# Kernel optimization log

Hardware: AMD Instinct MI355X
Metric: run time of the kernel (lower is better)

Reference implementation:

```python
import jax, jax.numpy as jnp
import numpy as np

EPS_PHI = 1e-18  # weight assigned to neighbors outside the support radius


def setup_inputs() -> dict:
    key = jax.random.key(0)
    k1, k2, k3, k4 = jax.random.split(key, 4)
    N, P, K = 2, 100000, 60
    points = jax.random.normal(k1, (N, P, 3), dtype=jnp.float32)
    v = jax.random.normal(k2, (N, P, K, 3), dtype=jnp.float32)
    vn = jax.random.normal(k3, (N, P, K, 3), dtype=jnp.float32)
    # squared support radii: positive, bounded away from zero
    sr = jax.random.uniform(k4, (N, P, K), dtype=jnp.float32) + 0.1
    return {"points": points, "v": v, "vn": vn, "sr": sr}


def reference(points, v, vn, sr):
    # points: (N,P,3); v,vn: (N,P,K,3); sr: (N,P,K)
    p_v = points[:, :, None, :] - v                      # (N,P,K,3)
    dists = jnp.sum(p_v * p_v, axis=-1)                  # (N,P,K) squared distances
    inside = dists < sr                                  # (N,P,K)
    w = 1.0 - dists / sr
    phi_v = jnp.where(inside, (w * w) * (w * w), EPS_PHI)  # quartic kernel weight
    v_to_p_dot_n = jnp.sum(vn * p_v, axis=-1)            # (N,P,K)
    sdf = jnp.sum(phi_v * v_to_p_dot_n, axis=-1) / jnp.sum(phi_v, axis=-1)  # (N,P)
    return jnp.sum(sdf * sdf, axis=-1)                   # (N,)
```

## Files before the change

### kernel.cpp

```cpp
#include <hip/hip_runtime.h>

#define RED_THREADS 512

__global__ __launch_bounds__(256) void sdf_main(
    const float* __restrict__ points,
    const float* __restrict__ v,
    const float* __restrict__ vn,
    const float* __restrict__ sr,
    float* __restrict__ ws,
    int NP, int P, int slots, int slotStride)
{
    constexpr int K = 60;
    __shared__ float4 sv[4][45];
    __shared__ float4 sn[4][45];
    __shared__ float4 ss[4][15];

    const int w     = threadIdx.x >> 6;
    const int lane  = threadIdx.x & 63;
    const int point = blockIdx.x * 4 + w;
    const bool active = point < NP;

    float px = 0.f, py = 0.f, pz = 0.f;
    if (active) {
        const float4* v4 = (const float4*)(v  + (size_t)point * (K * 3));
        const float4* n4 = (const float4*)(vn + (size_t)point * (K * 3));
        const float4* s4 = (const float4*)(sr + (size_t)point * K);
        float4 rv, rn, rs;
        if (lane < 45) rv = v4[lane];
        if (lane < 45) rn = n4[lane];
        if (lane < 15) rs = s4[lane];
        px = points[point * 3 + 0];
        py = points[point * 3 + 1];
        pz = points[point * 3 + 2];
        if (lane < 45) sv[w][lane] = rv;
        if (lane < 45) sn[w][lane] = rn;
        if (lane < 15) ss[w][lane] = rs;
    }
    __syncthreads();

    float num = 0.f, den = 0.f;
    if (active && lane < K) {
        const float* vf = (const float*)sv[w];
        const float* nf = (const float*)sn[w];
        const float* sf = (const float*)ss[w];
        const float vx = vf[3 * lane + 0];
        const float vy = vf[3 * lane + 1];
        const float vz = vf[3 * lane + 2];
        const float nx = nf[3 * lane + 0];
        const float ny = nf[3 * lane + 1];
        const float nz = nf[3 * lane + 2];
        const float s  = sf[lane];

        const float dx = px - vx;
        const float dy = py - vy;
        const float dz = pz - vz;
        const float d2 = dx * dx + dy * dy + dz * dz;
        const float wq = 1.0f - d2 / s;
        const float w2 = wq * wq;
        const float phi = (d2 < s) ? (w2 * w2) : 1e-18f;
        const float dot = nx * dx + ny * dy + nz * dz;
        num = phi * dot;
        den = phi;
    }

    #pragma unroll
    for (int off = 32; off >= 1; off >>= 1) {
        num += __shfl_xor(num, off, 64);
        den += __shfl_xor(den, off, 64);
    }

    if (active && lane == 0) {
        const float sdf = num / den;
        const int n    = point / P;
        const int slot = point & (slots - 1);
        atomicAdd(&ws[slot * slotStride + n], sdf * sdf);
    }
}

__global__ __launch_bounds__(RED_THREADS) void sdf_reduce(
    const float* __restrict__ ws, float* __restrict__ out,
    int N, int slots, int slotStride)
{
    __shared__ float sm0[RED_THREADS];
    __shared__ float sm1[RED_THREADS];
    const int tid = threadIdx.x;
    float a = 0.f, b = 0.f;
    for (int s = tid; s < slots; s += RED_THREADS) {
        a += ws[s * slotStride + 0];
        if (N > 1) b += ws[s * slotStride + 1];
    }
    sm0[tid] = a;
    sm1[tid] = b;
    __syncthreads();
    #pragma unroll
    for (int s = RED_THREADS / 2; s >= 1; s >>= 1) {
        if (tid < s) {
            sm0[tid] += sm0[tid + s];
            sm1[tid] += sm1[tid + s];
        }
        __syncthreads();
    }
    if (tid == 0) {
        out[0] = sm0[0];
        if (N > 1) out[1] = sm1[0];
    }
}

extern "C" void kernel_launch(void* const* d_in, const int* in_sizes, int n_in,
                              void* d_out, int out_size, void* d_ws, size_t ws_size,
                              hipStream_t stream) {
    const float* points = (const float*)d_in[0];
    const float* v      = (const float*)d_in[1];
    const float* vn     = (const float*)d_in[2];
    const float* sr     = (const float*)d_in[3];
    float* out = (float*)d_out;
    float* ws  = (float*)d_ws;

    const int NP = in_sizes[0] / 3;
    const int N  = out_size;
    const int P  = NP / N;

    int slots = 512, slotStride = 16;
    if (ws_size < (size_t)(slots * slotStride * sizeof(float))) {
        slots = 256; slotStride = 2;
    }

    hipMemsetAsync(ws, 0, (size_t)slots * slotStride * sizeof(float), stream);

    const int blocks = (NP + 3) / 4;
    sdf_main<<<blocks, 256, 0, stream>>>(points, v, vn, sr, ws, NP, P,
                                         slots, slotStride);
    sdf_reduce<<<1, RED_THREADS, 0, stream>>>(ws, out, N, slots, slotStride);
}
```

Before: 327.0 us.

## Use persistent waves with register-prefetched point groups and per-wave accumulation

Replaces the one-point-per-wave grid with a fixed grid of 1280 blocks. Each wave walks a contiguous range of points in groups of four, prefetching the next group's v/vn/sr into registers while computing the current group from shared memory. Per-batch partial sums are kept in registers and flushed with a few atomics per wave, cutting atomic traffic. The added block-level syncs and the serialized per-point shuffle reductions may limit how much latency is hidden. With cpw around 20, the final group per wave is partial.

```diff
diff --git a/kernel.cpp b/kernel.cpp
--- a/kernel.cpp
+++ b/kernel.cpp
@@ -1,79 +1,136 @@
 #include <hip/hip_runtime.h>
 
+#define WPB 4
+#define BT  256
+#define G   4
+#define MAXN 4
 #define RED_THREADS 512
 
-__global__ __launch_bounds__(256) void sdf_main(
+__global__ __launch_bounds__(BT) void sdf_main(
     const float* __restrict__ points,
     const float* __restrict__ v,
     const float* __restrict__ vn,
     const float* __restrict__ sr,
     float* __restrict__ ws,
-    int NP, int P, int slots, int slotStride)
+    int NP, int P, int cpw, int iters, int slots, int slotStride)
 {
-    constexpr int K = 60;
-    __shared__ float4 sv[4][45];
-    __shared__ float4 sn[4][45];
-    __shared__ float4 ss[4][15];
+    constexpr int K   = 60;
+    constexpr int VF4 = 45;
+    constexpr int SF4 = 15;
+    __shared__ float4 buf[WPB][G * (2 * VF4 + SF4)];
 
-    const int w     = threadIdx.x >> 6;
-    const int lane  = threadIdx.x & 63;
-    const int point = blockIdx.x * 4 + w;
-    const bool active = point < NP;
+    const int w      = threadIdx.x >> 6;
+    const int lane   = threadIdx.x & 63;
+    const int waveId = blockIdx.x * WPB + w;
+    const int p0     = waveId * cpw;
+    const int pEnd   = min(NP, p0 + cpw);
 
-    float px = 0.f, py = 0.f, pz = 0.f;
-    if (active) {
-        const float4* v4 = (const float4*)(v  + (size_t)point * (K * 3));
-        const float4* n4 = (const float4*)(vn + (size_t)point * (K * 3));
-        const float4* s4 = (const float4*)(sr + (size_t)point * K);
-        float4 rv, rn, rs;
-        if (lane < 45) rv = v4[lane];
-        if (lane < 45) rn = n4[lane];
-        if (lane < 15) rs = s4[lane];
-        px = points[point * 3 + 0];
-        py = points[point * 3 + 1];
-        pz = points[point * 3 + 2];
-        if (lane < 45) sv[w][lane] = rv;
-        if (lane < 45) sn[w][lane] = rn;
-        if (lane < 15) ss[w][lane] = rs;
-    }
-    __syncthreads();
+    float4* lv = &buf[w][0];
+    float4* ln = &buf[w][G * VF4];
+    float4* ls = &buf[w][2 * G * VF4];
 
-    float num = 0.f, den = 0.f;
-    if (active && lane < K) {
-        const float* vf = (const float*)sv[w];
-        const float* nf = (const float*)sn[w];
-        const float* sf = (const float*)ss[w];
-        const float vx = vf[3 * lane + 0];
-        const float vy = vf[3 * lane + 1];
-        const float vz = vf[3 * lane + 2];
-        const float nx = nf[3 * lane + 0];
-        const float ny = nf[3 * lane + 1];
-        const float nz = nf[3 * lane + 2];
-        const float s  = sf[lane];
+    float acc[MAXN];
+    #pragma unroll
+    for (int i = 0; i < MAXN; ++i) acc[i] = 0.f;
 
-        const float dx = px - vx;
-        const float dy = py - vy;
-        const float dz = pz - vz;
-        const float d2 = dx * dx + dy * dy + dz * dz;
-        const float wq = 1.0f - d2 / s;
-        const float w2 = wq * wq;
-        const float phi = (d2 < s) ? (w2 * w2) : 1e-18f;
-        const float dot = nx * dx + ny * dy + nz * dz;
-        num = phi * dot;
-        den = phi;
+    float4 z = {0.f, 0.f, 0.f, 0.f};
+    float4 rv0 = z, rv1 = z, rv2 = z, rn0 = z, rn1 = z, rn2 = z, rs0 = z;
+
+    {
+        const int npts = max(0, min(G, pEnd - p0));
+        const int nv = npts * VF4, ns = npts * SF4;
+        const float4* v4 = (const float4*)(v  + (size_t)p0 * (K * 3));
+        const float4* n4 = (const float4*)(vn + (size_t)p0 * (K * 3));
+        const float4* s4 = (const float4*)(sr + (size_t)p0 * K);
+        if (lane       < nv) rv0 = v4[lane];
+        if (lane +  64 < nv) rv1 = v4[lane + 64];
+        if (lane + 128 < nv) rv2 = v4[lane + 128];
+        if (lane       < nv) rn0 = n4[lane];
+        if (lane +  64 < nv) rn1 = n4[lane + 64];
+        if (lane + 128 < nv) rn2 = n4[lane + 128];
+        if (lane       < ns) rs0 = s4[lane];
     }
 
-    #pragma unroll
-    for (int off = 32; off >= 1; off >>= 1) {
-        num += __shfl_xor(num, off, 64);
-        den += __shfl_xor(den, off, 64);
+    for (int it = 0; it < iters; ++it) {
+        const int p    = p0 + it * G;
+        const int npts = max(0, min(G, pEnd - p));
+        const int nv = npts * VF4, ns = npts * SF4;
+
+        __syncthreads();
+        if (lane       < nv) lv[lane      ] = rv0;
+        if (lane +  64 < nv) lv[lane +  64] = rv1;
+        if (lane + 128 < nv) lv[lane + 128] = rv2;
+        if (lane       < nv) ln[lane      ] = rn0;
+        if (lane +  64 < nv) ln[lane +  64] = rn1;
+        if (lane + 128 < nv) ln[lane + 128] = rn2;
+        if (lane       < ns) ls[lane      ] = rs0;
+        __syncthreads();
+
+        {
+            const int pn = p + G;
+            const int nn = max(0, min(G, pEnd - pn));
+            const int nv2 = nn * VF4, ns2 = nn * SF4;
+            const float4* v4 = (const float4*)(v  + (size_t)pn * (K * 3));
+            const float4* n4 = (const float4*)(vn + (size_t)pn * (K * 3));
+            const float4* s4 = (const float4*)(sr + (size_t)pn * K);
+            if (lane       < nv2) rv0 = v4[lane];
+            if (lane +  64 < nv2) rv1 = v4[lane + 64];
+            if (lane + 128 < nv2) rv2 = v4[lane + 128];
+            if (lane       < nv2) rn0 = n4[lane];
+            if (lane +  64 < nv2) rn1 = n4[lane + 64];
+            if (lane + 128 < nv2) rn2 = n4[lane + 128];
+            if (lane       < ns2) rs0 = s4[lane];
+        }
+
+        const float* vf = (const float*)lv;
+        const float* nf = (const float*)ln;
+        const float* sf = (const float*)ls;
+
+        #pragma unroll
+        for (int g = 0; g < G; ++g) {
+            float num = 0.f, den = 0.f;
+            if (g < npts && lane < K) {
+                const int pt = p + g;
+                const float px = points[pt * 3 + 0];
+                const float py = points[pt * 3 + 1];
+                const float pz = points[pt * 3 + 2];
+                const float vx = vf[g * (VF4 * 4) + 3 * lane + 0];
+                const float vy = vf[g * (VF4 * 4) + 3 * lane + 1];
+                const float vz = vf[g * (VF4 * 4) + 3 * lane + 2];
+                const float nx = nf[g * (VF4 * 4) + 3 * lane + 0];
+                const float ny = nf[g * (VF4 * 4) + 3 * lane + 1];
+                const float nz = nf[g * (VF4 * 4) + 3 * lane + 2];
+                const float s  = sf[g * (SF4 * 4) + lane];
+
+                const float dx = px - vx;
+                const float dy = py - vy;
+                const float dz = pz - vz;
+                const float d2 = dx * dx + dy * dy + dz * dz;
+                const float wq = 1.0f - d2 / s;
+                const float w2 = wq * wq;
+                const float phi = (d2 < s) ? (w2 * w2) : 1e-18f;
+                const float dot = nx * dx + ny * dy + nz * dz;
+                num = phi * dot;
+                den = phi;
+            }
+            #pragma unroll
+            for (int off = 32; off >= 1; off >>= 1) {
+                num += __shfl_xor(num, off, 64);
+                den += __shfl_xor(den, off, 64);
+            }
+            if (lane == 0 && g < npts) {
+                const float sdf = num / den;
+                const int n = (p + g) / P;
+                if (n < MAXN) acc[n] += sdf * sdf;
+            }
+        }
     }
 
-    if (active && lane == 0) {
-        const float sdf = num / den;
-        const int n    = point / P;
-        const int slot = point & (slots - 1);
-        atomicAdd(&ws[slot * slotStride + n], sdf * sdf);
+    if (lane == 0) {
+        const int slot = waveId & (slots - 1);
+        #pragma unroll
+        for (int n = 0; n < MAXN; ++n)
+            if (acc[n] != 0.f) atomicAdd(&ws[slot * slotStride + n], acc[n]);
     }
 }
 
@@ -127,8 +184,12 @@
 
     hipMemsetAsync(ws, 0, (size_t)slots * slotStride * sizeof(float), stream);
 
-    const int blocks = (NP + 3) / 4;
-    sdf_main<<<blocks, 256, 0, stream>>>(points, v, vn, sr, ws, NP, P,
-                                         slots, slotStride);
+    const int blocks = 1280;
+    const int waves  = blocks * WPB;
+    const int cpw    = (NP + waves - 1) / waves;
+    const int iters  = (cpw + G - 1) / G;
+
+    sdf_main<<<blocks, BT, 0, stream>>>(points, v, vn, sr, ws,
+                                        NP, P, cpw, iters, slots, slotStride);
     sdf_reduce<<<1, RED_THREADS, 0, stream>>>(ws, out, N, slots, slotStride);
 }
```

Measured after the change: 345.7 us. 1.06x slower.

## Use grid-stride persistent waves with 16 lanes per point and per-wave accumulation

Applied to the files above, without the earlier changes.

The kernel becomes persistent: 2048 blocks grid-stride over groups of four points per wave. Each 16-lane subgroup handles one point, with four neighbors per lane loaded straight from global memory, so the shared-memory staging and the block barrier are gone. Per-point squared sdf values are accumulated in registers and reduced once per wave, which removes the per-point atomics. The division is replaced with a hardware reciprocal approximation, adding slight precision risk, and a generic fallback kernel is added for other K values.

```diff
diff --git a/kernel.cpp b/kernel.cpp
--- a/kernel.cpp
+++ b/kernel.cpp
@@ -1,80 +1,125 @@
 #include <hip/hip_runtime.h>
 
+#define BT  256
+#define WPB (BT / 64)
 #define RED_THREADS 512
+#define EPS_PHI 1e-18f
 
-__global__ __launch_bounds__(256) void sdf_main(
+__global__ __launch_bounds__(BT, 4) void sdf_main60(
     const float* __restrict__ points,
     const float* __restrict__ v,
     const float* __restrict__ vn,
     const float* __restrict__ sr,
     float* __restrict__ ws,
-    int NP, int P, int slots, int slotStride)
+    int P, int nGroups, int nWaves, int slots, int slotStride)
 {
-    constexpr int K = 60;
-    __shared__ float4 sv[4][45];
-    __shared__ float4 sn[4][45];
-    __shared__ float4 ss[4][15];
+    const int lane   = threadIdx.x & 63;
+    const int waveId = blockIdx.x * WPB + (threadIdx.x >> 6);
+    const int t = lane & 15;
+    const int g = lane >> 4;
 
-    const int w     = threadIdx.x >> 6;
-    const int lane  = threadIdx.x & 63;
-    const int point = blockIdx.x * 4 + w;
-    const bool active = point < NP;
+    const int  i3     = (t < 12) ? (144 + 3 * t) : 177;
+    const int  s3i    = (t < 12) ? (48 + t)      : 59;
+    const bool valid3 = (t < 12);
 
-    float px = 0.f, py = 0.f, pz = 0.f;
-    if (active) {
-        const float4* v4 = (const float4*)(v  + (size_t)point * (K * 3));
-        const float4* n4 = (const float4*)(vn + (size_t)point * (K * 3));
-        const float4* s4 = (const float4*)(sr + (size_t)point * K);
-        float4 rv, rn, rs;
-        if (lane < 45) rv = v4[lane];
-        if (lane < 45) rn = n4[lane];
-        if (lane < 15) rs = s4[lane];
-        px = points[point * 3 + 0];
-        py = points[point * 3 + 1];
-        pz = points[point * 3 + 2];
-        if (lane < 45) sv[w][lane] = rv;
-        if (lane < 45) sn[w][lane] = rn;
-        if (lane < 15) ss[w][lane] = rs;
-    }
-    __syncthreads();
+    float acc0 = 0.f, acc1 = 0.f;
 
-    float num = 0.f, den = 0.f;
-    if (active && lane < K) {
-        const float* vf = (const float*)sv[w];
-        const float* nf = (const float*)sn[w];
-        const float* sf = (const float*)ss[w];
-        const float vx = vf[3 * lane + 0];
-        const float vy = vf[3 * lane + 1];
-        const float vz = vf[3 * lane + 2];
-        const float nx = nf[3 * lane + 0];
-        const float ny = nf[3 * lane + 1];
-        const float nz = nf[3 * lane + 2];
-        const float s  = sf[lane];
+    for (int grp = waveId; grp < nGroups; grp += nWaves) {
+        const int p = grp * 4 + g;
+        const float* __restrict__ vrow = v      + (size_t)p * 180;
+        const float* __restrict__ nrow = vn     + (size_t)p * 180;
+        const float* __restrict__ srow = sr     + (size_t)p * 60;
+        const float* __restrict__ prow = points + (size_t)p * 3;
+        const int i0 = 3 * t;
 
-        const float dx = px - vx;
-        const float dy = py - vy;
-        const float dz = pz - vz;
-        const float d2 = dx * dx + dy * dy + dz * dz;
-        const float wq = 1.0f - d2 / s;
-        const float w2 = wq * wq;
-        const float phi = (d2 < s) ? (w2 * w2) : 1e-18f;
-        const float dot = nx * dx + ny * dy + nz * dz;
-        num = phi * dot;
-        den = phi;
+        const float vx0 = vrow[i0 +  0], vy0 = vrow[i0 +  1], vz0 = vrow[i0 +  2];
+        const float vx1 = vrow[i0 + 48], vy1 = vrow[i0 + 49], vz1 = vrow[i0 + 50];
+        const float vx2 = vrow[i0 + 96], vy2 = vrow[i0 + 97], vz2 = vrow[i0 + 98];
+        const float vx3 = vrow[i3 +  0], vy3 = vrow[i3 +  1], vz3 = vrow[i3 +  2];
+        const float nx0 = nrow[i0 +  0], ny0 = nrow[i0 +  1], nz0 = nrow[i0 +  2];
+        const float nx1 = nrow[i0 + 48], ny1 = nrow[i0 + 49], nz1 = nrow[i0 + 50];
+        const float nx2 = nrow[i0 + 96], ny2 = nrow[i0 + 97], nz2 = nrow[i0 + 98];
+        const float nx3 = nrow[i3 +  0], ny3 = nrow[i3 +  1], nz3 = nrow[i3 +  2];
+        const float s0 = srow[t], s1 = srow[t + 16], s2 = srow[t + 32], s3 = srow[s3i];
+        const float px = prow[0], py = prow[1], pz = prow[2];
+
+        float num = 0.f, den = 0.f;
+        auto body = [&](float vx, float vy, float vz,
+                        float nx, float ny, float nz,
+                        float s, bool valid) {
+            const float dx = px - vx, dy = py - vy, dz = pz - vz;
+            const float d2 = dx * dx + dy * dy + dz * dz;
+            const float rs = __builtin_amdgcn_rcpf(s);
+            const float w  = 1.f - d2 * rs;
+            const float w2 = w * w;
+            float phi = (d2 < s) ? (w2 * w2) : EPS_PHI;
+            if (!valid) phi = 0.f;
+            const float dot = nx * dx + ny * dy + nz * dz;
+            num += phi * dot;
+            den += phi;
+        };
+        body(vx0, vy0, vz0, nx0, ny0, nz0, s0, true);
+        body(vx1, vy1, vz1, nx1, ny1, nz1, s1, true);
+        body(vx2, vy2, vz2, nx2, ny2, nz2, s2, true);
+        body(vx3, vy3, vz3, nx3, ny3, nz3, s3, valid3);
+
+        #pragma unroll
+        for (int off = 1; off <= 8; off <<= 1) {
+            num += __shfl_xor(num, off, 64);
+            den += __shfl_xor(den, off, 64);
+        }
+
+        const float sdf = num * __builtin_amdgcn_rcpf(den);
+        const float sq  = sdf * sdf;
+        if (t == 0) {
+            if (p < P) acc0 += sq; else acc1 += sq;
+        }
     }
 
     #pragma unroll
-    for (int off = 32; off >= 1; off >>= 1) {
-        num += __shfl_xor(num, off, 64);
-        den += __shfl_xor(den, off, 64);
+    for (int off = 1; off <= 32; off <<= 1) {
+        acc0 += __shfl_xor(acc0, off, 64);
+        acc1 += __shfl_xor(acc1, off, 64);
     }
+    if (lane == 0) {
+        const int slot = waveId & (slots - 1);
+        atomicAdd(&ws[slot * slotStride + 0], acc0);
+        atomicAdd(&ws[slot * slotStride + 1], acc1);
+    }
+}
 
-    if (active && lane == 0) {
-        const float sdf = num / den;
-        const int n    = point / P;
-        const int slot = point & (slots - 1);
-        atomicAdd(&ws[slot * slotStride + n], sdf * sdf);
+__global__ void sdf_generic(
+    const float* __restrict__ points,
+    const float* __restrict__ v,
+    const float* __restrict__ vn,
+    const float* __restrict__ sr,
+    float* __restrict__ ws,
+    int NP, int P, int K, int slots, int slotStride)
+{
+    const int p = blockIdx.x * blockDim.x + threadIdx.x;
+    if (p >= NP) return;
+    const float px = points[p * 3 + 0];
+    const float py = points[p * 3 + 1];
+    const float pz = points[p * 3 + 2];
+    float num = 0.f, den = 0.f;
+    for (int k = 0; k < K; ++k) {
+        const size_t b = ((size_t)p * K + k) * 3;
+        const float dx = px - v[b + 0];
+        const float dy = py - v[b + 1];
+        const float dz = pz - v[b + 2];
+        const float d2 = dx * dx + dy * dy + dz * dz;
+        const float s  = sr[(size_t)p * K + k];
+        const float w  = 1.f - d2 / s;
+        const float w2 = w * w;
+        const float phi = (d2 < s) ? (w2 * w2) : EPS_PHI;
+        const float dot = vn[b + 0] * dx + vn[b + 1] * dy + vn[b + 2] * dz;
+        num += phi * dot;
+        den += phi;
     }
+    const float sdf = num / den;
+    const int n = p / P;
+    const int slot = p & (slots - 1);
+    if (n < slotStride) atomicAdd(&ws[slot * slotStride + n], sdf * sdf);
 }
 
 __global__ __launch_bounds__(RED_THREADS) void sdf_reduce(
@@ -117,6 +162,7 @@
     float* ws  = (float*)d_ws;
 
     const int NP = in_sizes[0] / 3;
+    const int K  = in_sizes[3] / NP;
     const int N  = out_size;
     const int P  = NP / N;
 
@@ -127,8 +173,16 @@
 
     hipMemsetAsync(ws, 0, (size_t)slots * slotStride * sizeof(float), stream);
 
-    const int blocks = (NP + 3) / 4;
-    sdf_main<<<blocks, 256, 0, stream>>>(points, v, vn, sr, ws, NP, P,
-                                         slots, slotStride);
+    if (K == 60 && (NP & 3) == 0) {
+        const int blocks  = 2048;
+        const int nWaves  = blocks * WPB;
+        const int nGroups = NP / 4;
+        sdf_main60<<<blocks, BT, 0, stream>>>(points, v, vn, sr, ws,
+                                              P, nGroups, nWaves,
+                                              slots, slotStride);
+    } else {
+        sdf_generic<<<(NP + BT - 1) / BT, BT, 0, stream>>>(
+            points, v, vn, sr, ws, NP, P, K, slots, slotStride);
+    }
     sdf_reduce<<<1, RED_THREADS, 0, stream>>>(ws, out, N, slots, slotStride);
 }
```

After: 333.6 us. 2.0% more time.
